# Optimization experiments

Measured on AMD Instinct MI355X. Metric: run time of the kernel, lower is better.

Reference implementation:

```python
import jax, jax.numpy as jnp
import numpy as np

D = 512          # hidden_dim
NH = 8           # num_heads
DH = D // NH     # head dim
N = 100000       # num_nodes
C = 64           # context size
E = 1600000      # num_edges (unused in math, required by signature)
LN_EPS = 1e-5


def layer_norm(x, g, b):
    mu = jnp.mean(x, axis=-1, keepdims=True)
    var = jnp.var(x, axis=-1, keepdims=True)
    return (x - mu) * jax.lax.rsqrt(var + LN_EPS) * g + b


def mha(q, kv, W_in, b_in, W_out, b_out):
    # torch nn.MultiheadAttention (batch of 1 folded out). q:[Lq,D], kv:[Lk,D]
    Wq, Wk, Wv = jnp.split(W_in, 3, axis=0)
    bq, bk, bv = jnp.split(b_in, 3)
    qh = (q @ Wq.T + bq).reshape(-1, NH, DH)
    kh = (kv @ Wk.T + bk).reshape(-1, NH, DH)
    vh = (kv @ Wv.T + bv).reshape(-1, NH, DH)
    scores = jnp.einsum('qhd,khd->hqk', qh, kh) * (DH ** -0.5)
    w = jax.nn.softmax(scores, axis=-1)
    out = jnp.einsum('hqk,khd->qhd', w, vh).reshape(-1, D)
    return out @ W_out.T + b_out


def setup_inputs() -> dict:
    key = jax.random.key(0)
    ks = jax.random.split(key, 12)
    s = 0.02
    return {
        'H': jax.random.normal(ks[0], (N, D), jnp.float32),
        'path_token': jax.random.normal(ks[1], (D,), jnp.float32),
        'W_in1': jax.random.normal(ks[2], (3 * D, D), jnp.float32) * s,
        'b_in1': jnp.zeros((3 * D,), jnp.float32),
        'W_out1': jax.random.normal(ks[3], (D, D), jnp.float32) * s,
        'b_out1': jnp.zeros((D,), jnp.float32),
        'W_in2': jax.random.normal(ks[4], (3 * D, D), jnp.float32) * s,
        'b_in2': jnp.zeros((3 * D,), jnp.float32),
        'W_out2': jax.random.normal(ks[5], (D, D), jnp.float32) * s,
        'b_out2': jnp.zeros((D,), jnp.float32),
        'ln1_g': jnp.ones((D,), jnp.float32),
        'ln1_b': jnp.zeros((D,), jnp.float32),
        'ln2_g': jnp.ones((D,), jnp.float32),
        'ln2_b': jnp.zeros((D,), jnp.float32),
        'edge_index': jax.random.randint(ks[6], (2, E), 0, N, jnp.int64)
            if jax.config.jax_enable_x64 else jax.random.randint(ks[6], (2, E), 0, N, jnp.int32),
        'context_ids': jax.random.randint(ks[7], (C,), 0, N, jnp.int32),
    }


def reference(H, path_token, W_in1, b_in1, W_out1, b_out1,
              W_in2, b_in2, W_out2, b_out2,
              ln1_g, ln1_b, ln2_g, ln2_b,
              edge_index, context_ids):
    # gather context node reprs [C, D]
    ctx = H[context_ids]
    # path attention: 1 query (path token) over C context keys/values
    upd = mha(path_token[None, :], ctx, W_in1, b_in1, W_out1, b_out1)[0]
    upd = layer_norm(upd + path_token, ln1_g, ln1_b)  # [D]
    # graph attention: every node queries N identical copies of `upd`.
    # All logits per query are equal -> softmax exactly uniform -> per-head
    # output == v_head(upd). So attn_out = out_proj(v_proj(upd)), identical
    # for every node (exact, not approximate).
    _, _, Wv2 = jnp.split(W_in2, 3, axis=0)
    bv2 = b_in2[2 * D:]
    v = upd @ Wv2.T + bv2                       # [D]
    attn2 = v @ W_out2.T + b_out2               # [D], broadcast over nodes
    H_cond = layer_norm(attn2[None, :] + H, ln2_g, ln2_b)  # [N, D]
    return H_cond
```

## Files before the change

kernel.cpp:

```cpp
#include <hip/hip_runtime.h>

#define D 512
#define NH 8
#define DH 64
#define CCTX 64
#define LN_EPS 1e-5f
#define NCHAIN 128
#define FROWS  25

#define WS_T     0
#define WS_M     512
#define WS_CTX   5120
#define WS_CBAR  40960
#define WS_O     45056
#define WS_OUT1  45568
#define WS_V     46080
#define WS_ATTN2 46592
#define WS_FLAGS 47104

typedef float f4v __attribute__((ext_vector_type(4)));

__device__ __forceinline__ float waveReduceSum(float v) {
#pragma unroll
    for (int off = 32; off > 0; off >>= 1) v += __shfl_xor(v, off);
    return v;
}

__device__ __forceinline__ void barFlags(unsigned* flags, unsigned phase) {
    __syncthreads();
    if (threadIdx.x == 0)
        __hip_atomic_store(&flags[blockIdx.x], phase, __ATOMIC_RELEASE,
                           __HIP_MEMORY_SCOPE_AGENT);
    if (threadIdx.x < 64) {
        while (true) {
            unsigned f0 = __hip_atomic_load(&flags[threadIdx.x],
                                            __ATOMIC_RELAXED, __HIP_MEMORY_SCOPE_AGENT);
            unsigned f1 = __hip_atomic_load(&flags[64 + threadIdx.x],
                                            __ATOMIC_RELAXED, __HIP_MEMORY_SCOPE_AGENT);
            if (__all(f0 >= phase && f1 >= phase)) break;
            __builtin_amdgcn_s_sleep(2);
        }
        __builtin_amdgcn_fence(__ATOMIC_ACQUIRE, "agent");
    }
    __syncthreads();
}

__global__ __launch_bounds__(128) void k_init(unsigned* flags) {
    flags[threadIdx.x] = 0u;
}

__device__ __forceinline__ void matvec_rows(
    const float* __restrict__ W, const float* __restrict__ x,
    const float* __restrict__ b, float* __restrict__ y, int headStride)
{
    int wib = threadIdx.x >> 6, lane = threadIdx.x & 63;
    int r = blockIdx.x * 4 + wib;
    const float* xr = x + (r >> 6) * headStride;
    const float* Wr = W + (size_t)r * D;
    float4 w0 = *(const float4*)(Wr + lane * 4);
    float4 w1 = *(const float4*)(Wr + 256 + lane * 4);
    float4 x0 = *(const float4*)(xr + lane * 4);
    float4 x1 = *(const float4*)(xr + 256 + lane * 4);
    float s = w0.x*x0.x + w0.y*x0.y + w0.z*x0.z + w0.w*x0.w
            + w1.x*x1.x + w1.y*x1.y + w1.z*x1.z + w1.w*x1.w;
    s = waveReduceSum(s);
    if (lane == 0) y[r] = s + b[r];
}

__global__ __launch_bounds__(256) void k_chain(
    const float* __restrict__ Hm,   const float* __restrict__ path,
    const float* __restrict__ Win1, const float* __restrict__ bin1,
    const float* __restrict__ Wout1,const float* __restrict__ bout1,
    const float* __restrict__ Win2, const float* __restrict__ bin2,
    const float* __restrict__ Wout2,const float* __restrict__ bout2,
    const float* __restrict__ ln1g, const float* __restrict__ ln1b,
    const int* __restrict__ ids,    float* __restrict__ ws)
{
    __shared__ __align__(16) float smem[532];
    unsigned* flags = (unsigned*)(ws + WS_FLAGS);
    const int B = blockIdx.x, tid = threadIdx.x;
    const int wib = tid >> 6, lane = tid & 63;

    if (B < 64) {
        if (tid < 128) {
            int id = ids[B];
            float4 v = *(const float4*)(Hm + (size_t)id * D + tid * 4);
            *(float4*)(ws + WS_CTX + B * D + tid * 4) = v;
        }
    } else if (B < 80) {
        int bm = B - 64;
        int h = bm >> 1, half = bm & 1;
        float* qh_lds = smem;
        {
            int rr = tid >> 2, p = tid & 3;
            const float* wrow = Win1 + (size_t)(h * DH + rr) * D + p * 128;
            const float* xrow = path + p * 128;
            float s = 0.f;
#pragma unroll 8
            for (int k = 0; k < 32; ++k) {
                float4 a = *(const float4*)(wrow + k * 4);
                float4 c = *(const float4*)(xrow + k * 4);
                s += a.x*c.x + a.y*c.y + a.z*c.z + a.w*c.w;
            }
            s += __shfl_xor(s, 1);
            s += __shfl_xor(s, 2);
            if (p == 0) qh_lds[rr] = s + bin1[h * DH + rr];
        }
        __syncthreads();
        {
            int c = half * 256 + tid;
            const float* Wk = Win1 + (size_t)D * D;
            float acc = 0.f;
#pragma unroll 8
            for (int d = 0; d < DH; ++d)
                acc += Wk[(size_t)(h * DH + d) * D + c] * qh_lds[d];
            ws[WS_M + h * D + c] = acc;
        }
        if (half == 0 && tid == 0) {
            float tt = 0.f;
            for (int d = 0; d < DH; ++d) tt += bin1[D + h * DH + d] * qh_lds[d];
            ws[WS_T + h] = tt;
        }
    }
    barFlags(flags, 1);

    if (B < NH) {
        const int h = B;
        float* s_lds = smem;
        float* w_lds = smem + 64;
        {
            int j = tid >> 2, p = tid & 3;
            const float* cr = ws + WS_CTX + j * D + p * 128;
            const float* mr = ws + WS_M + h * D + p * 128;
            float s = 0.f;
#pragma unroll 8
            for (int c4 = 0; c4 < 32; ++c4) {
                float4 a = *(const float4*)(cr + c4 * 4);
                float4 b = *(const float4*)(mr + c4 * 4);
                s += a.x*b.x + a.y*b.y + a.z*b.z + a.w*b.w;
            }
            s += __shfl_xor(s, 1);
            s += __shfl_xor(s, 2);
            if (p == 0) s_lds[j] = (s + ws[WS_T + h]) * 0.125f;
        }
        __syncthreads();
        if (wib == 0) {
            float sc = s_lds[lane];
            float mx = sc;
#pragma unroll
            for (int off = 32; off > 0; off >>= 1) mx = fmaxf(mx, __shfl_xor(mx, off));
            float e = __expf(sc - mx);
            float sum = waveReduceSum(e);
            w_lds[lane] = e / sum;
        }
        __syncthreads();
        for (int c = tid; c < D; c += 256) {
            float acc = 0.f;
#pragma unroll 8
            for (int j = 0; j < CCTX; ++j) acc += w_lds[j] * ws[WS_CTX + j * D + c];
            ws[WS_CBAR + h * D + c] = acc;
        }
    }
    barFlags(flags, 2);

    matvec_rows(Win1 + 2 * (size_t)D * D, ws + WS_CBAR, bin1 + 2 * D, ws + WS_O, D);
    barFlags(flags, 3);

    matvec_rows(Wout1, ws + WS_O, bout1, ws + WS_OUT1, 0);
    barFlags(flags, 4);

    {
        float* xs  = smem;
        float* red = smem + 520;
        float a0 = ws[WS_OUT1 + tid * 2]     + path[tid * 2];
        float a1 = ws[WS_OUT1 + tid * 2 + 1] + path[tid * 2 + 1];
        float s  = a0 + a1;
        float s2 = a0 * a0 + a1 * a1;
        s  = waveReduceSum(s);
        s2 = waveReduceSum(s2);
        if (lane == 0) { red[wib] = s; red[4 + wib] = s2; }
        __syncthreads();
        float st  = red[0] + red[1] + red[2] + red[3];
        float s2t = red[4] + red[5] + red[6] + red[7];
        float mu   = st * (1.f / D);
        float var  = s2t * (1.f / D) - mu * mu;
        float rinv = rsqrtf(var + LN_EPS);
        xs[tid * 2]     = (a0 - mu) * rinv * ln1g[tid * 2]     + ln1b[tid * 2];
        xs[tid * 2 + 1] = (a1 - mu) * rinv * ln1g[tid * 2 + 1] + ln1b[tid * 2 + 1];
        __syncthreads();
        matvec_rows(Win2 + 2 * (size_t)D * D, xs, bin2 + 2 * D, ws + WS_V, 0);
    }
    barFlags(flags, 5);

    matvec_rows(Wout2, ws + WS_V, bout2, ws + WS_ATTN2, 0);
}

__global__ __launch_bounds__(256) void k_final(
    const float* __restrict__ Hm, const float* __restrict__ attn2,
    const float* __restrict__ g, const float* __restrict__ b,
    float* __restrict__ out, int N)
{
    __shared__ __align__(16) float tile[FROWS * D];
    __shared__ float murinv[FROWS * 2];
    const int tid  = threadIdx.x;
    const int lane = tid & 63, wib = tid >> 6;
    const int rstart = blockIdx.x * FROWS;
    const int nrows  = (rstart + FROWS <= N) ? FROWS : (N - rstart);
    if (nrows <= 0) return;
    const int nf4 = nrows * (D / 4);

    const f4v*   H4 = (const f4v*)Hm;
    f4v*         O4 = (f4v*)out;
    float4*      T4 = (float4*)tile;
    const size_t base4 = (size_t)rstart * (D / 4);

    const int col4 = tid & 127;
    float4 av = ((const float4*)attn2)[col4];
    float4 gv = ((const float4*)g)[col4];
    float4 bv = ((const float4*)b)[col4];
    float4 a0 = ((const float4*)attn2)[lane];
    float4 a1 = ((const float4*)attn2)[64 + lane];

#pragma unroll 4
    for (int i = tid; i < nf4; i += 256) {
        f4v v = __builtin_nontemporal_load(H4 + base4 + i);
        float4 f; f.x = v.x; f.y = v.y; f.z = v.z; f.w = v.w;
        T4[i] = f;
    }
    __syncthreads();

    for (int r = wib; r < nrows; r += 4) {
        float4 x0 = T4[r * 128 + lane];
        float4 x1 = T4[r * 128 + 64 + lane];
        float e0x = x0.x + a0.x, e0y = x0.y + a0.y, e0z = x0.z + a0.z, e0w = x0.w + a0.w;
        float e1x = x1.x + a1.x, e1y = x1.y + a1.y, e1z = x1.z + a1.z, e1w = x1.w + a1.w;
        float s  = e0x + e0y + e0z + e0w + e1x + e1y + e1z + e1w;
        float s2 = e0x*e0x + e0y*e0y + e0z*e0z + e0w*e0w
                 + e1x*e1x + e1y*e1y + e1z*e1z + e1w*e1w;
#pragma unroll
        for (int off = 32; off > 0; off >>= 1) {
            s  += __shfl_xor(s,  off);
            s2 += __shfl_xor(s2, off);
        }
        float mu   = s * (1.f / D);
        float var  = s2 * (1.f / D) - mu * mu;
        float rinv = rsqrtf(var + LN_EPS);
        if (lane == 0) { murinv[r * 2] = mu; murinv[r * 2 + 1] = rinv; }
    }
    __syncthreads();

#pragma unroll 4
    for (int i = tid; i < nf4; i += 256) {
        int r = i >> 7;
        float4 x   = T4[i];
        float mu   = murinv[r * 2];
        float rinv = murinv[r * 2 + 1];
        f4v y;
        y.x = (x.x + av.x - mu) * rinv * gv.x + bv.x;
        y.y = (x.y + av.y - mu) * rinv * gv.y + bv.y;
        y.z = (x.z + av.z - mu) * rinv * gv.z + bv.z;
        y.w = (x.w + av.w - mu) * rinv * gv.w + bv.w;
        __builtin_nontemporal_store(y, O4 + base4 + i);
    }
}

extern "C" void kernel_launch(void* const* d_in, const int* in_sizes, int n_in,
                              void* d_out, int out_size, void* d_ws, size_t ws_size,
                              hipStream_t stream)
{
    const float* Hm    = (const float*)d_in[0];
    const float* path  = (const float*)d_in[1];
    const float* Win1  = (const float*)d_in[2];
    const float* bin1  = (const float*)d_in[3];
    const float* Wout1 = (const float*)d_in[4];
    const float* bout1 = (const float*)d_in[5];
    const float* Win2  = (const float*)d_in[6];
    const float* bin2  = (const float*)d_in[7];
    const float* Wout2 = (const float*)d_in[8];
    const float* bout2 = (const float*)d_in[9];
    const float* ln1g  = (const float*)d_in[10];
    const float* ln1b  = (const float*)d_in[11];
    const float* ln2g  = (const float*)d_in[12];
    const float* ln2b  = (const float*)d_in[13];
    const int*   ids   = (const int*)d_in[15];

    float* ws  = (float*)d_ws;
    float* out = (float*)d_out;
    const int N = in_sizes[0] / D;
    const int FB = (N + FROWS - 1) / FROWS;

    k_init<<<1, 128, 0, stream>>>((unsigned*)(ws + WS_FLAGS));
    k_chain<<<NCHAIN, 256, 0, stream>>>(Hm, path, Win1, bin1, Wout1, bout1,
                                        Win2, bin2, Wout2, bout2, ln1g, ln1b,
                                        ids, ws);
    k_final<<<FB, 256, 0, stream>>>(Hm, ws + WS_ATTN2, ln2g, ln2b, out, N);
}
```

Baseline: 134.4 us.

## Make final LayerNorm kernel persistent with grid-wide barriers between load and store phases

Replaces the one-block-per-25-rows launch of the final LayerNorm kernel with a fixed grid of 768 persistent blocks that loop over rounds of row tiles. A flag-based grid barrier now separates each round's read/statistics phase from its write phase, and another separates consecutive rounds, so all blocks read from HBM together and then write together. The H loads switch from nontemporal to normal loads. Each round adds two spin barriers over 768 flags, and the scheme needs all 768 blocks to be co-resident or it will deadlock.

```diff
diff --git a/kernel.cpp b/kernel.cpp
--- a/kernel.cpp
+++ b/kernel.cpp
@@ -7,16 +7,18 @@
 #define LN_EPS 1e-5f
 #define NCHAIN 128
 #define FROWS  25
-
-#define WS_T     0
-#define WS_M     512
-#define WS_CTX   5120
-#define WS_CBAR  40960
-#define WS_O     45056
-#define WS_OUT1  45568
-#define WS_V     46080
-#define WS_ATTN2 46592
-#define WS_FLAGS 47104
+#define NFB    768
+
+#define WS_T      0
+#define WS_M      512
+#define WS_CTX    5120
+#define WS_CBAR   40960
+#define WS_O      45056
+#define WS_OUT1   45568
+#define WS_V      46080
+#define WS_ATTN2  46592
+#define WS_FLAGS  47104
+#define WS_FLAGS2 47232
 
 typedef float f4v __attribute__((ext_vector_type(4)));
 
@@ -45,8 +47,31 @@
     __syncthreads();
 }
 
-__global__ __launch_bounds__(128) void k_init(unsigned* flags) {
-    flags[threadIdx.x] = 0u;
+__device__ __forceinline__ void barFinal(unsigned* f2, unsigned phase) {
+    __syncthreads();
+    if (threadIdx.x == 0)
+        __hip_atomic_store(&f2[blockIdx.x], phase, __ATOMIC_RELEASE,
+                           __HIP_MEMORY_SCOPE_AGENT);
+    if (threadIdx.x < 64) {
+        while (true) {
+            bool ok = true;
+#pragma unroll
+            for (int k = 0; k < NFB / 64; ++k) {
+                unsigned v = __hip_atomic_load(&f2[threadIdx.x + k * 64],
+                                               __ATOMIC_RELAXED, __HIP_MEMORY_SCOPE_AGENT);
+                ok &= (v >= phase);
+            }
+            if (__all(ok)) break;
+            __builtin_amdgcn_s_sleep(1);
+        }
+    }
+    __syncthreads();
+}
+
+__global__ __launch_bounds__(1024) void k_init(unsigned* flags) {
+    if (threadIdx.x < 128) flags[threadIdx.x] = 0u;
+    unsigned* f2 = flags + (WS_FLAGS2 - WS_FLAGS);
+    if (threadIdx.x < NFB) f2[threadIdx.x] = 0u;
 }
 
 __device__ __forceinline__ void matvec_rows(
@@ -198,21 +223,17 @@
 __global__ __launch_bounds__(256) void k_final(
     const float* __restrict__ Hm, const float* __restrict__ attn2,
     const float* __restrict__ g, const float* __restrict__ b,
-    float* __restrict__ out, int N)
+    float* __restrict__ out, int N, int rounds, unsigned* __restrict__ f2)
 {
     __shared__ __align__(16) float tile[FROWS * D];
     __shared__ float murinv[FROWS * 2];
     const int tid  = threadIdx.x;
     const int lane = tid & 63, wib = tid >> 6;
-    const int rstart = blockIdx.x * FROWS;
-    const int nrows  = (rstart + FROWS <= N) ? FROWS : (N - rstart);
-    if (nrows <= 0) return;
-    const int nf4 = nrows * (D / 4);
+    const int B = blockIdx.x;
 
     const f4v*   H4 = (const f4v*)Hm;
     f4v*         O4 = (f4v*)out;
     float4*      T4 = (float4*)tile;
-    const size_t base4 = (size_t)rstart * (D / 4);
 
     const int col4 = tid & 127;
     float4 av = ((const float4*)attn2)[col4];
@@ -221,46 +242,65 @@
     float4 a0 = ((const float4*)attn2)[lane];
     float4 a1 = ((const float4*)attn2)[64 + lane];
 
+    unsigned phase = 0;
+    for (int rd = 0; rd < rounds; ++rd) {
+        const int rstart = (rd * NFB + B) * FROWS;
+        const int nrows  = (rstart >= N) ? 0
+                          : ((rstart + FROWS <= N) ? FROWS : (N - rstart));
+        const int nf4 = nrows * (D / 4);
+        const size_t base4 = (size_t)rstart * (D / 4);
+
+        if (nrows > 0) {
 #pragma unroll 4
-    for (int i = tid; i < nf4; i += 256) {
-        f4v v = __builtin_nontemporal_load(H4 + base4 + i);
-        float4 f; f.x = v.x; f.y = v.y; f.z = v.z; f.w = v.w;
-        T4[i] = f;
-    }
-    __syncthreads();
-
-    for (int r = wib; r < nrows; r += 4) {
-        float4 x0 = T4[r * 128 + lane];
-        float4 x1 = T4[r * 128 + 64 + lane];
-        float e0x = x0.x + a0.x, e0y = x0.y + a0.y, e0z = x0.z + a0.z, e0w = x0.w + a0.w;
-        float e1x = x1.x + a1.x, e1y = x1.y + a1.y, e1z = x1.z + a1.z, e1w = x1.w + a1.w;
-        float s  = e0x + e0y + e0z + e0w + e1x + e1y + e1z + e1w;
-        float s2 = e0x*e0x + e0y*e0y + e0z*e0z + e0w*e0w
-                 + e1x*e1x + e1y*e1y + e1z*e1z + e1w*e1w;
+            for (int i = tid; i < nf4; i += 256) {
+                f4v v = H4[base4 + i];
+                float4 f; f.x = v.x; f.y = v.y; f.z = v.z; f.w = v.w;
+                T4[i] = f;
+            }
+        }
+        __syncthreads();
+        if (nrows > 0) {
+            for (int r = wib; r < nrows; r += 4) {
+                float4 x0 = T4[r * 128 + lane];
+                float4 x1 = T4[r * 128 + 64 + lane];
+                float e0x = x0.x + a0.x, e0y = x0.y + a0.y, e0z = x0.z + a0.z, e0w = x0.w + a0.w;
+                float e1x = x1.x + a1.x, e1y = x1.y + a1.y, e1z = x1.z + a1.z, e1w = x1.w + a1.w;
+                float s  = e0x + e0y + e0z + e0w + e1x + e1y + e1z + e1w;
+                float s2 = e0x*e0x + e0y*e0y + e0z*e0z + e0w*e0w
+                         + e1x*e1x + e1y*e1y + e1z*e1z + e1w*e1w;
 #pragma unroll
-        for (int off = 32; off > 0; off >>= 1) {
-            s  += __shfl_xor(s,  off);
-            s2 += __shfl_xor(s2, off);
-        }
-        float mu   = s * (1.f / D);
-        float var  = s2 * (1.f / D) - mu * mu;
-        float rinv = rsqrtf(var + LN_EPS);
-        if (lane == 0) { murinv[r * 2] = mu; murinv[r * 2 + 1] = rinv; }
-    }
-    __syncthreads();
-
+                for (int off = 32; off > 0; off >>= 1) {
+                    s  += __shfl_xor(s,  off);
+                    s2 += __shfl_xor(s2, off);
+                }
+                float mu   = s * (1.f / D);
+                float var  = s2 * (1.f / D) - mu * mu;
+                float rinv = rsqrtf(var + LN_EPS);
+                if (lane == 0) { murinv[r * 2] = mu; murinv[r * 2 + 1] = rinv; }
+            }
+        }
+        ++phase;
+        barFinal(f2, phase);
+
+        if (nrows > 0) {
 #pragma unroll 4
-    for (int i = tid; i < nf4; i += 256) {
-        int r = i >> 7;
-        float4 x   = T4[i];
-        float mu   = murinv[r * 2];
-        float rinv = murinv[r * 2 + 1];
-        f4v y;
-        y.x = (x.x + av.x - mu) * rinv * gv.x + bv.x;
-        y.y = (x.y + av.y - mu) * rinv * gv.y + bv.y;
-        y.z = (x.z + av.z - mu) * rinv * gv.z + bv.z;
-        y.w = (x.w + av.w - mu) * rinv * gv.w + bv.w;
-        __builtin_nontemporal_store(y, O4 + base4 + i);
+            for (int i = tid; i < nf4; i += 256) {
+                int r = i >> 7;
+                float4 x   = T4[i];
+                float mu   = murinv[r * 2];
+                float rinv = murinv[r * 2 + 1];
+                f4v y;
+                y.x = (x.x + av.x - mu) * rinv * gv.x + bv.x;
+                y.y = (x.y + av.y - mu) * rinv * gv.y + bv.y;
+                y.z = (x.z + av.z - mu) * rinv * gv.z + bv.z;
+                y.w = (x.w + av.w - mu) * rinv * gv.w + bv.w;
+                __builtin_nontemporal_store(y, O4 + base4 + i);
+            }
+        }
+        if (rd + 1 < rounds) {
+            ++phase;
+            barFinal(f2, phase);
+        }
     }
 }
 
@@ -287,11 +327,12 @@
     float* ws  = (float*)d_ws;
     float* out = (float*)d_out;
     const int N = in_sizes[0] / D;
-    const int FB = (N + FROWS - 1) / FROWS;
-
-    k_init<<<1, 128, 0, stream>>>((unsigned*)(ws + WS_FLAGS));
+    const int rounds = (N + NFB * FROWS - 1) / (NFB * FROWS);
+
+    k_init<<<1, 1024, 0, stream>>>((unsigned*)(ws + WS_FLAGS));
     k_chain<<<NCHAIN, 256, 0, stream>>>(Hm, path, Win1, bin1, Wout1, bout1,
                                         Win2, bin2, Wout2, bout2, ln1g, ln1b,
                                         ids, ws);
-    k_final<<<FB, 256, 0, stream>>>(Hm, ws + WS_ATTN2, ln2g, ln2b, out, N);
-}
+    k_final<<<NFB, 256, 0, stream>>>(Hm, ws + WS_ATTN2, ln2g, ln2b, out, N,
+                                     rounds, (unsigned*)(ws + WS_FLAGS2));
+}
```

Result: slower. 375.9 us (+179.7%).
